# Optimization experiments

Measured on AMD Instinct MI355X. Metric: run time of the kernel, lower is better.

Reference implementation:

```python
import jax, jax.numpy as jnp
import numpy as np

DIM = 256
HEADS = 8
DIM_HEAD = 64
INNER = HEADS * DIM_HEAD  # 512
B, N = 4, 1024


def setup_inputs() -> dict:
    key = jax.random.key(0)
    ks = jax.random.split(key, 7)
    x = jax.random.normal(ks[0], (B, N, DIM), dtype=jnp.float32)
    attn_bias = jax.random.normal(ks[1], (B, HEADS, N, N), dtype=jnp.float32)
    s = 1.0 / np.sqrt(DIM)
    Wq = jax.random.normal(ks[2], (DIM, INNER), dtype=jnp.float32) * s
    Wkv = jax.random.normal(ks[3], (DIM, 2 * INNER), dtype=jnp.float32) * s
    # to_out initialized to zero in the torch module; use small random so output is non-trivial
    Wo = jax.random.normal(ks[4], (INNER, DIM), dtype=jnp.float32) * (1.0 / np.sqrt(INNER))
    bo = jnp.zeros((DIM,), dtype=jnp.float32)
    # gating initialized weight=0, bias=1 -> sigmoid(1); use small random weight + bias 1
    Wg = jax.random.normal(ks[5], (DIM, INNER), dtype=jnp.float32) * 0.02
    bg = jnp.ones((INNER,), dtype=jnp.float32)
    return {"x": x, "attn_bias": attn_bias, "Wq": Wq, "Wkv": Wkv,
            "Wo": Wo, "bo": bo, "Wg": Wg, "bg": bg}


def reference(x, attn_bias, Wq, Wkv, Wo, bo, Wg, bg):
    b, n, _ = x.shape
    scale = DIM_HEAD ** -0.5
    q = x @ Wq                                    # [b, n, inner]
    kv = x @ Wkv                                  # [b, n, 2*inner]
    k, v = jnp.split(kv, 2, axis=-1)
    def split_heads(t):
        return t.reshape(b, n, HEADS, DIM_HEAD).transpose(0, 2, 1, 3)  # [b,h,n,d]
    q, k, v = split_heads(q) * scale, split_heads(k), split_heads(v)
    dots = jnp.einsum('bhid,bhjd->bhij', q, k) + attn_bias
    # explicit max-subtract then softmax (matches original; numerically identical)
    attn = jax.nn.softmax(dots, axis=-1)
    out = jnp.einsum('bhij,bhjd->bhid', attn, v)  # [b,h,n,d]
    out = out.transpose(0, 2, 1, 3).reshape(b, n, INNER)
    gates = jax.nn.sigmoid(x @ Wg + bg)
    out = out * gates
    return out @ Wo + bo
```

## Files before the change

kernel.cpp:

```cpp
#include <hip/hip_runtime.h>

typedef unsigned short u16;
typedef unsigned int u32;
typedef __attribute__((ext_vector_type(8))) __bf16 bf16x8;
typedef __attribute__((ext_vector_type(4))) float floatx4;
typedef const __attribute__((address_space(1))) unsigned char glob_u8;
typedef __attribute__((address_space(3))) unsigned char lds_u8;

#define DEV __device__ __forceinline__

DEV u16 f2bf(float f) {
  return __builtin_bit_cast(u16, (__bf16)f);
}
DEV float bf2f(u16 h) {
  u32 u = ((u32)h) << 16;
  return __builtin_bit_cast(float, u);
}
DEV floatx4 MFMA(bf16x8 a, bf16x8 b, floatx4 c) {
  return __builtin_amdgcn_mfma_f32_16x16x32_bf16(a, b, c, 0, 0, 0);
}

__global__ void convert_k(const float* __restrict__ x, const float* __restrict__ Wq,
                          const float* __restrict__ Wkv, const float* __restrict__ Wg,
                          const float* __restrict__ Wo,
                          u16* __restrict__ xA, u16* __restrict__ WB, u16* __restrict__ WoT) {
  int i = blockIdx.x * 256 + threadIdx.x;
  if (i < 131072) {
    int tile = i >> 9, w = i & 511;
    int g = w >> 6, q = (w >> 4) & 3, l15 = w & 15;
    int rb = tile >> 3, kb = tile & 7;
    int row = rb * 128 + g * 16 + l15;
    int k0 = kb * 32 + q * 8;
    float4 v0 = *(const float4*)(x + row * 256 + k0);
    float4 v1 = *(const float4*)(x + row * 256 + k0 + 4);
    u16 o[8] = {f2bf(v0.x), f2bf(v0.y), f2bf(v0.z), f2bf(v0.w),
                f2bf(v1.x), f2bf(v1.y), f2bf(v1.z), f2bf(v1.w)};
    *(uint4*)(xA + (size_t)i * 8) = *(uint4*)o;
    return;
  }
  i -= 131072;
  if (i < 65536) {
    int tile = i >> 8, w = i & 255;
    int g = (w >> 6) & 3, q = (w >> 4) & 3, l15 = w & 15;
    int nb = tile >> 3, kb = tile & 7;
    int n = nb * 64 + g * 16 + l15;
    int k0 = kb * 32 + q * 8;
    u16 o[8];
#pragma unroll
    for (int e = 0; e < 8; ++e) {
      int k = k0 + e;
      float v;
      if (n < 512) v = Wq[k * 512 + n];
      else if (n < 1536) v = Wkv[k * 1024 + (n - 512)];
      else v = Wg[k * 512 + (n - 1536)];
      o[e] = f2bf(v);
    }
    *(uint4*)(WB + (size_t)i * 8) = *(uint4*)o;
    return;
  }
  i -= 65536;
  if (i < 131072) {
    int n = i >> 9, kk = i & 511;
    WoT[i] = f2bf(Wo[kk * 256 + n]);
  }
}

__global__ __launch_bounds__(256, 4) void gemm_qkvg(
    const u16* __restrict__ xA, const u16* __restrict__ WB, const float* __restrict__ bg,
    u16* __restrict__ qb, u16* __restrict__ kfrag, u16* __restrict__ vfrag, u16* __restrict__ gb) {
  __shared__ __attribute__((aligned(16))) u16 As[2][4096];
  __shared__ __attribute__((aligned(16))) u16 Bs[2][2048];
  const int tid = threadIdx.x;
  const int wave = tid >> 6, lane = tid & 63;
  const int lane15 = lane & 15, quad = lane >> 4;
  const int rb = blockIdx.x;
  const int nb = blockIdx.y;
  const int rm0 = rb * 128;
  const int cn0 = nb * 64;
  const int wm = (wave & 1) * 64, wn = (wave >> 1) * 32;
  const int ga = (wave & 1) * 4;
  const int gb2 = (wave >> 1) * 2;

  floatx4 acc[4][2] = {};

  auto stage = [&](int kb, int bufi) {
    const u16* At = xA + ((size_t)(rb * 8 + kb)) * 4096;
    const u16* Bt = WB + ((size_t)(nb * 8 + kb)) * 2048;
#pragma unroll
    for (int c = 0; c < 2; ++c) {
      int ch = wave * 2 + c;
      __builtin_amdgcn_global_load_lds((glob_u8*)(At + ch * 512 + lane * 8),
                                       (lds_u8*)(&As[bufi][ch * 512]), 16, 0, 0);
    }
    __builtin_amdgcn_global_load_lds((glob_u8*)(Bt + wave * 512 + lane * 8),
                                     (lds_u8*)(&Bs[bufi][wave * 512]), 16, 0, 0);
  };

  stage(0, 0);
  __syncthreads();
  int cur = 0;
#pragma unroll 1
  for (int kb = 0; kb < 8; ++kb) {
    if (kb < 7) stage(kb + 1, cur ^ 1);
    const u16* Ac = As[cur];
    const u16* Bc = Bs[cur];
    bf16x8 af[4], bfr[2];
#pragma unroll
    for (int mt = 0; mt < 4; ++mt) af[mt] = *(const bf16x8*)(Ac + ((ga + mt) * 64 + lane) * 8);
#pragma unroll
    for (int nt = 0; nt < 2; ++nt) bfr[nt] = *(const bf16x8*)(Bc + ((gb2 + nt) * 64 + lane) * 8);
#pragma unroll
    for (int mt = 0; mt < 4; ++mt)
#pragma unroll
      for (int nt = 0; nt < 2; ++nt)
        acc[mt][nt] = MFMA(af[mt], bfr[nt], acc[mt][nt]);
    __syncthreads();
    cur ^= 1;
  }
#pragma unroll
  for (int mt = 0; mt < 4; ++mt)
#pragma unroll
    for (int nt = 0; nt < 2; ++nt)
#pragma unroll
      for (int r = 0; r < 4; ++r) {
        int row = rm0 + wm + mt * 16 + quad * 4 + r;
        int col = cn0 + wn + nt * 16 + lane15;
        float v = acc[mt][nt][r];
        int b = row >> 10, n = row & 1023;
        if (col < 512) {
          int h = col >> 6, d = col & 63;
          qb[((b * 8 + h) * 1024 + n) * 64 + d] = f2bf(v * 0.125f);
        } else if (col < 1024) {
          int c = col - 512, h = c >> 6, d = c & 63;
          int bh2 = b * 8 + h;
          int t = n >> 4, l15 = n & 15;
          int half = d >> 5, qd = (d >> 3) & 3, e = d & 7;
          kfrag[(size_t)bh2 * 65536 + t * 1024 + half * 512 + (qd * 16 + l15) * 8 + e] = f2bf(v);
        } else if (col < 1536) {
          int c = col - 1024, h = c >> 6, d = c & 63;
          int bh2 = b * 8 + h;
          int t64 = n >> 6, ck = (n >> 5) & 1, qd = (n >> 3) & 3, e = n & 7;
          int dt = d >> 4, l15 = d & 15;
          vfrag[(size_t)bh2 * 65536 + t64 * 4096 + dt * 1024 + ck * 512 + (qd * 16 + l15) * 8 + e] = f2bf(v);
        } else {
          int c = col - 1536;
          float g = 1.0f / (1.0f + __expf(-(v + bg[c])));
          gb[row * 512 + c] = f2bf(g);
        }
      }
}

__global__ __launch_bounds__(256, 4) void attn_k(
    const u16* __restrict__ qb, const u16* __restrict__ kfrag, const u16* __restrict__ vfrag,
    const float* __restrict__ bias, const u16* __restrict__ gb, u16* __restrict__ ogb) {
  __shared__ __attribute__((aligned(16))) u16 Kt[2][4096];
  __shared__ __attribute__((aligned(16))) u16 Vt[2][4096];
  __shared__ __attribute__((aligned(16))) u16 Ps[4 * 16 * 40];
  const int tid = threadIdx.x;
  const int wave = tid >> 6, lane = tid & 63;
  const int lane15 = lane & 15, quad = lane >> 4;
  const int bh = blockIdx.x;
  const int q0 = blockIdx.y * 32;
  const int qw = (wave & 1) * 16;
  const int kh = wave >> 1;

  bf16x8 qf0, qf1;
  {
    const u16* qrow = qb + ((size_t)(bh * 1024 + q0 + qw + lane15)) * 64 + quad * 8;
    qf0 = *(const bf16x8*)(qrow);
    qf1 = *(const bf16x8*)(qrow + 32);
  }
  bf16x8 ones;
#pragma unroll
  for (int e = 0; e < 8; ++e) ones[e] = __builtin_bit_cast(__bf16, (u16)0x3F80);

  floatx4 oacc[4] = {};
  floatx4 lacc = {};

  u16* Pw = Ps + wave * (16 * 40);
  const u16* kp = kfrag + (size_t)bh * 65536;
  const u16* vp = vfrag + (size_t)bh * 65536;
  const float* bbase = bias + ((size_t)(bh * 1024 + q0 + qw + quad * 4)) * 1024 + kh * 32 + lane15;

  auto stage = [&](int kt, int bufi) {
    const u16* kS = kp + kt * 4096;
    const u16* vS = vp + kt * 4096;
#pragma unroll
    for (int c = 0; c < 2; ++c) {
      int ch = wave * 2 + c;
      __builtin_amdgcn_global_load_lds((glob_u8*)(kS + ch * 512 + lane * 8),
                                       (lds_u8*)(&Kt[bufi][ch * 512]), 16, 0, 0);
      __builtin_amdgcn_global_load_lds((glob_u8*)(vS + ch * 512 + lane * 8),
                                       (lds_u8*)(&Vt[bufi][ch * 512]), 16, 0, 0);
    }
  };

  stage(0, 0);
  __syncthreads();
  int cur = 0;
#pragma unroll 1
  for (int kt = 0; kt < 16; ++kt) {
    if (kt < 15) stage(kt + 1, cur ^ 1);
    float bv[4][2];
#pragma unroll
    for (int r = 0; r < 4; ++r)
#pragma unroll
      for (int j = 0; j < 2; ++j)
        bv[r][j] = bbase[r * 1024 + kt * 64 + j * 16];
    const u16* Ktc = Kt[cur];
    const u16* Vtc = Vt[cur];
    floatx4 s[2];
#pragma unroll
    for (int j = 0; j < 2; ++j) {
      const u16* kb = Ktc + (kh * 2 + j) * 1024 + lane * 8;
      bf16x8 kf0 = *(const bf16x8*)(kb);
      bf16x8 kf1 = *(const bf16x8*)(kb + 512);
      floatx4 z = {};
      z = MFMA(qf0, kf0, z);
      s[j] = MFMA(qf1, kf1, z);
    }
#pragma unroll
    for (int j = 0; j < 2; ++j)
#pragma unroll
      for (int r = 0; r < 4; ++r)
        s[j][r] = __expf(s[j][r] + bv[r][j] - 8.0f);
#pragma unroll
    for (int j = 0; j < 2; ++j)
#pragma unroll
      for (int r = 0; r < 4; ++r)
        Pw[(quad * 4 + r) * 40 + j * 16 + lane15] = f2bf(s[j][r]);
    bf16x8 pf = *(const bf16x8*)(Pw + lane15 * 40 + quad * 8);

    lacc = MFMA(pf, ones, lacc);
#pragma unroll
    for (int dt = 0; dt < 4; ++dt) {
      bf16x8 vf = *(const bf16x8*)(Vtc + dt * 1024 + kh * 512 + lane * 8);
      oacc[dt] = MFMA(pf, vf, oacc[dt]);
    }
    __syncthreads();
    cur ^= 1;
  }

  float* red = (float*)Kt;
  if (wave >= 2) {
    float* r0 = red + (wave - 2) * 1280 + lane * 20;
#pragma unroll
    for (int dt = 0; dt < 4; ++dt)
#pragma unroll
      for (int r = 0; r < 4; ++r) r0[dt * 4 + r] = oacc[dt][r];
#pragma unroll
    for (int r = 0; r < 4; ++r) r0[16 + r] = lacc[r];
  }
  __syncthreads();
  if (wave < 2) {
    const float* r0 = red + wave * 1280 + lane * 20;
#pragma unroll
    for (int dt = 0; dt < 4; ++dt)
#pragma unroll
      for (int r = 0; r < 4; ++r) oacc[dt][r] += r0[dt * 4 + r];
#pragma unroll
    for (int r = 0; r < 4; ++r) lacc[r] += r0[16 + r];

    const int b = bh >> 3, h = bh & 7;
#pragma unroll
    for (int r = 0; r < 4; ++r) {
      int q = q0 + wave * 16 + quad * 4 + r;
      float inv = 1.0f / lacc[r];
      size_t base = ((size_t)(b * 1024 + q)) * 512 + h * 64;
#pragma unroll
      for (int dt = 0; dt < 4; ++dt) {
        size_t gi = base + dt * 16 + lane15;
        ogb[gi] = f2bf(oacc[dt][r] * inv * bf2f(gb[gi]));
      }
    }
  }
}

__global__ __launch_bounds__(256, 4) void gemm_out_k(
    const u16* __restrict__ og, const u16* __restrict__ WoT,
    const float* __restrict__ bo, float* __restrict__ out) {
  __shared__ __attribute__((aligned(16))) u16 As[64 * 40];
  __shared__ __attribute__((aligned(16))) u16 Bs[64 * 40];
  const int tid = threadIdx.x;
  const int wave = tid >> 6, lane = tid & 63;
  const int lane15 = lane & 15, quad = lane >> 4;
  const int rm0 = blockIdx.x * 64;
  const int cn0 = blockIdx.y * 64;
  const int wm = (wave & 1) * 32, wn = (wave >> 1) * 32;
  const int rowA = tid >> 2, segA = (tid & 3) * 8;
  floatx4 acc[2][2] = {};
  uint4 a0 = *(const uint4*)(og + (rm0 + rowA) * 512 + segA);
  uint4 b0 = *(const uint4*)(WoT + (cn0 + rowA) * 512 + segA);
#pragma unroll 1
  for (int k0 = 0; k0 < 512; k0 += 32) {
    __syncthreads();
    *(uint4*)(As + rowA * 40 + segA) = a0;
    *(uint4*)(Bs + rowA * 40 + segA) = b0;
    __syncthreads();
    if (k0 < 480) {
      a0 = *(const uint4*)(og + (rm0 + rowA) * 512 + k0 + 32 + segA);
      b0 = *(const uint4*)(WoT + (cn0 + rowA) * 512 + k0 + 32 + segA);
    }
    bf16x8 af[2], bfr[2];
#pragma unroll
    for (int mt = 0; mt < 2; ++mt) af[mt] = *(const bf16x8*)(As + (wm + mt * 16 + lane15) * 40 + quad * 8);
#pragma unroll
    for (int nt = 0; nt < 2; ++nt) bfr[nt] = *(const bf16x8*)(Bs + (wn + nt * 16 + lane15) * 40 + quad * 8);
#pragma unroll
    for (int mt = 0; mt < 2; ++mt)
#pragma unroll
      for (int nt = 0; nt < 2; ++nt)
        acc[mt][nt] = MFMA(af[mt], bfr[nt], acc[mt][nt]);
  }
#pragma unroll
  for (int nt = 0; nt < 2; ++nt) {
    int col = cn0 + wn + nt * 16 + lane15;
    float bv = bo[col];
#pragma unroll
    for (int mt = 0; mt < 2; ++mt)
#pragma unroll
      for (int r = 0; r < 4; ++r) {
        int row = rm0 + wm + mt * 16 + quad * 4 + r;
        out[(size_t)row * 256 + col] = acc[mt][nt][r] + bv;
      }
  }
}

extern "C" void kernel_launch(void* const* d_in, const int* in_sizes, int n_in,
                              void* d_out, int out_size, void* d_ws, size_t ws_size,
                              hipStream_t stream) {
  const float* x = (const float*)d_in[0];
  const float* bias = (const float*)d_in[1];
  const float* Wq = (const float*)d_in[2];
  const float* Wkv = (const float*)d_in[3];
  const float* Wo = (const float*)d_in[4];
  const float* bo = (const float*)d_in[5];
  const float* Wg = (const float*)d_in[6];
  const float* bg = (const float*)d_in[7];
  float* out = (float*)d_out;
  char* ws = (char*)d_ws;
  u16* xA    = (u16*)(ws);
  u16* WB    = (u16*)(ws + 2097152);
  u16* WoT   = (u16*)(ws + 3145728);
  u16* qb    = (u16*)(ws + 3407872);
  u16* kfrag = (u16*)(ws + 7602176);
  u16* vfrag = (u16*)(ws + 11796480);
  u16* gb    = (u16*)(ws + 15990784);
  u16* ogb   = (u16*)(ws + 20185088);

  convert_k<<<1280, 256, 0, stream>>>(x, Wq, Wkv, Wg, Wo, xA, WB, WoT);
  dim3 g1(32, 32);
  gemm_qkvg<<<g1, 256, 0, stream>>>(xA, WB, bg, qb, kfrag, vfrag, gb);
  dim3 g2(32, 32);
  attn_k<<<g2, 256, 0, stream>>>(qb, kfrag, vfrag, bias, gb, ogb);
  dim3 g3(64, 4);
  gemm_out_k<<<g3, 256, 0, stream>>>(ogb, WoT, bo, out);
}
```

Baseline: 248.0 us.

## Store gated attention output and Wo in MFMA fragment layout for direct LDS loads

The attention epilogue now writes the gated output in a pre-tiled MFMA fragment order, and the convert kernel writes Wo in a matching fragment layout. The output GEMM uses global_load_lds to move these tiles straight into double-buffered LDS, with 64x32 tiles and twice as many blocks. This removes register staging and the padded LDS layout, and convert launches fewer blocks. The cost is scattered 2-byte stores in the attention epilogue and a smaller per-block tile in the output GEMM.

```diff
diff --git a/kernel.cpp b/kernel.cpp
--- a/kernel.cpp
+++ b/kernel.cpp
@@ -23,7 +23,7 @@
 __global__ void convert_k(const float* __restrict__ x, const float* __restrict__ Wq,
                           const float* __restrict__ Wkv, const float* __restrict__ Wg,
                           const float* __restrict__ Wo,
-                          u16* __restrict__ xA, u16* __restrict__ WB, u16* __restrict__ WoT) {
+                          u16* __restrict__ xA, u16* __restrict__ WB, u16* __restrict__ WoF) {
   int i = blockIdx.x * 256 + threadIdx.x;
   if (i < 131072) {
     int tile = i >> 9, w = i & 511;
@@ -59,9 +59,16 @@
     return;
   }
   i -= 65536;
-  if (i < 131072) {
-    int n = i >> 9, kk = i & 511;
-    WoT[i] = f2bf(Wo[kk * 256 + n]);
+  if (i < 16384) {
+    int tile = i >> 7, w = i & 127;
+    int g = (w >> 6) & 1, q = (w >> 4) & 3, l15 = w & 15;
+    int nb32 = tile >> 4, kb = tile & 15;
+    int n = nb32 * 32 + g * 16 + l15;
+    int k0 = kb * 32 + q * 8;
+    u16 o[8];
+#pragma unroll
+    for (int e = 0; e < 8; ++e) o[e] = f2bf(Wo[(k0 + e) * 256 + n]);
+    *(uint4*)(WoF + (size_t)i * 8) = *(uint4*)o;
   }
 }
 
@@ -152,7 +159,7 @@
 
 __global__ __launch_bounds__(256, 4) void attn_k(
     const u16* __restrict__ qb, const u16* __restrict__ kfrag, const u16* __restrict__ vfrag,
-    const float* __restrict__ bias, const u16* __restrict__ gb, u16* __restrict__ ogb) {
+    const float* __restrict__ bias, const u16* __restrict__ gb, u16* __restrict__ ogf) {
   __shared__ __attribute__((aligned(16))) u16 Kt[2][4096];
   __shared__ __attribute__((aligned(16))) u16 Vt[2][4096];
   __shared__ __attribute__((aligned(16))) u16 Ps[4 * 16 * 40];
@@ -265,65 +272,73 @@
 #pragma unroll
     for (int r = 0; r < 4; ++r) {
       int q = q0 + wave * 16 + quad * 4 + r;
+      int row = b * 1024 + q;
       float inv = 1.0f / lacc[r];
-      size_t base = ((size_t)(b * 1024 + q)) * 512 + h * 64;
+      int rb64 = row >> 6, g = (row >> 4) & 3, l15r = row & 15;
 #pragma unroll
       for (int dt = 0; dt < 4; ++dt) {
-        size_t gi = base + dt * 16 + lane15;
-        ogb[gi] = f2bf(oacc[dt][r] * inv * bf2f(gb[gi]));
+        int k = h * 64 + dt * 16 + lane15;
+        size_t gi = ((size_t)row) * 512 + k;
+        int kb = k >> 5, qf = (k >> 3) & 3, e = k & 7;
+        ogf[((size_t)(rb64 * 16 + kb)) * 2048 + ((g * 4 + qf) * 16 + l15r) * 8 + e] =
+            f2bf(oacc[dt][r] * inv * bf2f(gb[gi]));
       }
     }
   }
 }
 
 __global__ __launch_bounds__(256, 4) void gemm_out_k(
-    const u16* __restrict__ og, const u16* __restrict__ WoT,
+    const u16* __restrict__ ogf, const u16* __restrict__ WoF,
     const float* __restrict__ bo, float* __restrict__ out) {
-  __shared__ __attribute__((aligned(16))) u16 As[64 * 40];
-  __shared__ __attribute__((aligned(16))) u16 Bs[64 * 40];
+  __shared__ __attribute__((aligned(16))) u16 As[2][2048];
+  __shared__ __attribute__((aligned(16))) u16 Bs[2][1024];
   const int tid = threadIdx.x;
   const int wave = tid >> 6, lane = tid & 63;
   const int lane15 = lane & 15, quad = lane >> 4;
-  const int rm0 = blockIdx.x * 64;
-  const int cn0 = blockIdx.y * 64;
-  const int wm = (wave & 1) * 32, wn = (wave >> 1) * 32;
-  const int rowA = tid >> 2, segA = (tid & 3) * 8;
-  floatx4 acc[2][2] = {};
-  uint4 a0 = *(const uint4*)(og + (rm0 + rowA) * 512 + segA);
-  uint4 b0 = *(const uint4*)(WoT + (cn0 + rowA) * 512 + segA);
+  const int rb = blockIdx.x;
+  const int nb = blockIdx.y;
+  const int ga = (wave & 1) * 2;
+  const int gbb = wave >> 1;
+
+  floatx4 acc[2] = {};
+
+  auto stage = [&](int kb, int bufi) {
+    const u16* At = ogf + ((size_t)(rb * 16 + kb)) * 2048;
+    __builtin_amdgcn_global_load_lds((glob_u8*)(At + wave * 512 + lane * 8),
+                                     (lds_u8*)(&As[bufi][wave * 512]), 16, 0, 0);
+    if (wave < 2) {
+      const u16* Bt = WoF + ((size_t)(nb * 16 + kb)) * 1024;
+      __builtin_amdgcn_global_load_lds((glob_u8*)(Bt + wave * 512 + lane * 8),
+                                       (lds_u8*)(&Bs[bufi][wave * 512]), 16, 0, 0);
+    }
+  };
+
+  stage(0, 0);
+  __syncthreads();
+  int cur = 0;
 #pragma unroll 1
-  for (int k0 = 0; k0 < 512; k0 += 32) {
+  for (int kb = 0; kb < 16; ++kb) {
+    if (kb < 15) stage(kb + 1, cur ^ 1);
+    const u16* Ac = As[cur];
+    const u16* Bc = Bs[cur];
+    bf16x8 af[2];
+#pragma unroll
+    for (int mt = 0; mt < 2; ++mt) af[mt] = *(const bf16x8*)(Ac + ((ga + mt) * 64 + lane) * 8);
+    bf16x8 bfr = *(const bf16x8*)(Bc + (gbb * 64 + lane) * 8);
+#pragma unroll
+    for (int mt = 0; mt < 2; ++mt) acc[mt] = MFMA(af[mt], bfr, acc[mt]);
     __syncthreads();
-    *(uint4*)(As + rowA * 40 + segA) = a0;
-    *(uint4*)(Bs + rowA * 40 + segA) = b0;
-    __syncthreads();
-    if (k0 < 480) {
-      a0 = *(const uint4*)(og + (rm0 + rowA) * 512 + k0 + 32 + segA);
-      b0 = *(const uint4*)(WoT + (cn0 + rowA) * 512 + k0 + 32 + segA);
-    }
-    bf16x8 af[2], bfr[2];
-#pragma unroll
-    for (int mt = 0; mt < 2; ++mt) af[mt] = *(const bf16x8*)(As + (wm + mt * 16 + lane15) * 40 + quad * 8);
-#pragma unroll
-    for (int nt = 0; nt < 2; ++nt) bfr[nt] = *(const bf16x8*)(Bs + (wn + nt * 16 + lane15) * 40 + quad * 8);
-#pragma unroll
-    for (int mt = 0; mt < 2; ++mt)
-#pragma unroll
-      for (int nt = 0; nt < 2; ++nt)
-        acc[mt][nt] = MFMA(af[mt], bfr[nt], acc[mt][nt]);
-  }
-#pragma unroll
-  for (int nt = 0; nt < 2; ++nt) {
-    int col = cn0 + wn + nt * 16 + lane15;
-    float bv = bo[col];
-#pragma unroll
-    for (int mt = 0; mt < 2; ++mt)
-#pragma unroll
-      for (int r = 0; r < 4; ++r) {
-        int row = rm0 + wm + mt * 16 + quad * 4 + r;
-        out[(size_t)row * 256 + col] = acc[mt][nt][r] + bv;
-      }
-  }
+    cur ^= 1;
+  }
+  const int col = nb * 32 + gbb * 16 + lane15;
+  const float bv = bo[col];
+#pragma unroll
+  for (int mt = 0; mt < 2; ++mt)
+#pragma unroll
+    for (int r = 0; r < 4; ++r) {
+      int row = rb * 64 + (wave & 1) * 32 + mt * 16 + quad * 4 + r;
+      out[(size_t)row * 256 + col] = acc[mt][r] + bv;
+    }
 }
 
 extern "C" void kernel_launch(void* const* d_in, const int* in_sizes, int n_in,
@@ -341,18 +356,18 @@
   char* ws = (char*)d_ws;
   u16* xA    = (u16*)(ws);
   u16* WB    = (u16*)(ws + 2097152);
-  u16* WoT   = (u16*)(ws + 3145728);
+  u16* WoF   = (u16*)(ws + 3145728);
   u16* qb    = (u16*)(ws + 3407872);
   u16* kfrag = (u16*)(ws + 7602176);
   u16* vfrag = (u16*)(ws + 11796480);
   u16* gb    = (u16*)(ws + 15990784);
-  u16* ogb   = (u16*)(ws + 20185088);
-
-  convert_k<<<1280, 256, 0, stream>>>(x, Wq, Wkv, Wg, Wo, xA, WB, WoT);
+  u16* ogf   = (u16*)(ws + 20185088);
+
+  convert_k<<<832, 256, 0, stream>>>(x, Wq, Wkv, Wg, Wo, xA, WB, WoF);
   dim3 g1(32, 32);
   gemm_qkvg<<<g1, 256, 0, stream>>>(xA, WB, bg, qb, kfrag, vfrag, gb);
   dim3 g2(32, 32);
-  attn_k<<<g2, 256, 0, stream>>>(qb, kfrag, vfrag, bias, gb, ogb);
-  dim3 g3(64, 4);
-  gemm_out_k<<<g3, 256, 0, stream>>>(ogb, WoT, bo, out);
-}
+  attn_k<<<g2, 256, 0, stream>>>(qb, kfrag, vfrag, bias, gb, ogf);
+  dim3 g3(64, 8);
+  gemm_out_k<<<g3, 256, 0, stream>>>(ogf, WoF, bo, out);
+}
```

New measurement: 250.4 us. Within noise of the previous version (+0.9%).
